# Kernel tuning notes

Measured on AMD Instinct MI355X. Metric: run time of the kernel, lower is better.

## Reference

```python
import jax, jax.numpy as jnp
import numpy as np

B, N, NODE_DIM, EMB, T = 16, 256, 5, 128, 4


def _linear_params(key, din, dout):
    kw, kb = jax.random.split(key)
    s = 1.0 / np.sqrt(din)
    w = jax.random.uniform(kw, (din, dout), minval=-s, maxval=s, dtype=jnp.float32)
    b = jax.random.uniform(kb, (dout,), minval=-s, maxval=s, dtype=jnp.float32)
    return w, b


def setup_inputs() -> dict:
    key = jax.random.key(0)
    ks = jax.random.split(key, 10)
    inp = {
        "xv": jax.random.normal(ks[0], (B, N, NODE_DIM), dtype=jnp.float32),
        "Ws": jax.random.uniform(ks[1], (B, N, N), dtype=jnp.float32),
    }
    inp["t1_w"], inp["t1_b"] = _linear_params(ks[2], NODE_DIM, EMB)
    inp["t2_w"], inp["t2_b"] = _linear_params(ks[3], EMB, EMB)
    inp["t3_w"], inp["t3_b"] = _linear_params(ks[4], EMB, EMB)
    inp["t4_w"], inp["t4_b"] = _linear_params(ks[5], 1, EMB)
    inp["t5_w"], inp["t5_b"] = _linear_params(ks[6], 2 * EMB, 1)
    inp["t6_w"], inp["t6_b"] = _linear_params(ks[7], EMB, EMB)
    inp["t7_w"], inp["t7_b"] = _linear_params(ks[8], EMB, EMB)
    inp["layer_w"], inp["layer_b"] = _linear_params(ks[9], EMB, EMB)
    return inp


def reference(xv, Ws, t1_w, t1_b, t2_w, t2_b, t3_w, t3_b, t4_w, t4_b,
              t5_w, t5_b, t6_w, t6_b, t7_w, t7_b, layer_w, layer_b):
    batch, num_nodes = xv.shape[0], xv.shape[1]
    emb = t1_w.shape[1]
    conn = (Ws > 0).astype(xv.dtype)  # [B,N,N]
    # s1 = layer(relu(theta1(xv)))
    s1 = jnp.maximum(xv @ t1_w + t1_b, 0.0) @ layer_w + layer_b  # [B,N,E]
    # s3 = theta3(sum_i relu(theta4(Ws[:,i,j,None])))
    s3_1 = jnp.maximum(Ws[..., None] * t4_w[0] + t4_b, 0.0)  # [B,N,N,E]
    s3 = s3_1.sum(axis=1) @ t3_w + t3_b  # [B,N,E]
    mu = jnp.zeros((batch, num_nodes, emb), dtype=xv.dtype)
    for _ in range(T):
        s2 = jnp.matmul(conn, mu) @ t2_w + t2_b  # [B,N,E]
        mu = jnp.maximum(s1 + s2 + s3, 0.0)
    # global state: theta6 applied to pooled mu, broadcast to all nodes
    global_state = mu.sum(axis=1, keepdims=True) @ t6_w + t6_b  # [B,1,E]
    global_state = jnp.broadcast_to(global_state, mu.shape)  # [B,N,E]
    local_action = mu @ t7_w + t7_b  # [B,N,E]
    out = jnp.maximum(jnp.concatenate([global_state, local_action], axis=2), 0.0)
    return (out @ t5_w + t5_b).squeeze(2)  # [B,N]
```

## Files before the change

kernel.cpp:

```cpp
#include <hip/hip_runtime.h>

#define BATCH 16
#define NN    256
#define E     128
#define NR    (BATCH*NN)
#define ZCAP  8

typedef float f4 __attribute__((ext_vector_type(4)));


__global__ __launch_bounds__(1024) void k_p1(
    const float* __restrict__ xv,  const float* __restrict__ Ws,
    const float* __restrict__ t1w, const float* __restrict__ t1b,
    const float* __restrict__ t3w, const float* __restrict__ t3b,
    const float* __restrict__ t4w, const float* __restrict__ t4b,
    const float* __restrict__ lw,  const float* __restrict__ lb,
    float* __restrict__ s13g, int* __restrict__ zcnt)
{
    const int blk = blockIdx.x;
    const int b   = blk >> 4;
    const int bt  = blk & 15;
    const int j0  = bt * 16;
    const int r0  = b*NN + j0;
    const int t   = threadIdx.x;
    const int e   = t & 127;
    const int q   = t >> 7;
    const int w   = t >> 6;
    const int l   = t & 63;

    __shared__ __align__(16) float s3p[2][16][E];
    __shared__ __align__(16) float s3l[16][E];
    __shared__ __align__(16) float hsl[16][E];
    __shared__ int lcnt[16];

    const float* wb = Ws + (size_t)b*NN*NN;

    {
        float b1 = t1b[e];
        float w0=t1w[e],w1=t1w[E+e],w2=t1w[2*E+e],w3=t1w[3*E+e],w4=t1w[4*E+e];
        #pragma unroll
        for (int rr = 0; rr < 2; ++rr) {
            const float* x = xv + (size_t)(r0 + q*2 + rr)*5;
            hsl[q*2+rr][e] =
                fmaxf(b1 + x[0]*w0+x[1]*w1+x[2]*w2+x[3]*w3+x[4]*w4, 0.f);
        }
    }
    {
        f4 v = *(const f4*)(wb + (size_t)(j0 + w)*NN + l*4);
        int c = (v.x<=0.f) + (v.y<=0.f) + (v.z<=0.f) + (v.w<=0.f);
        #pragma unroll
        for (int off = 32; off; off >>= 1) c += __shfl_down(c, off, 64);
        if (l == 0) lcnt[w] = c;
    }
    {
        const int cq = q & 3, ih = q >> 2;
        const float a = t4w[e], c = t4b[e];
        const float* wcol = wb + (size_t)(ih*128)*NN + j0 + cq*4;
        float x0=0.f, x1=0.f, x2=0.f, x3=0.f;
        #pragma unroll 8
        for (int i = 0; i < 128; ++i) {
            f4 wv = *(const f4*)(wcol + (size_t)i*NN);
            x0 += fmaxf(wv.x*a + c, 0.f);
            x1 += fmaxf(wv.y*a + c, 0.f);
            x2 += fmaxf(wv.z*a + c, 0.f);
            x3 += fmaxf(wv.w*a + c, 0.f);
        }
        s3p[ih][cq*4+0][e] = x0;
        s3p[ih][cq*4+1][e] = x1;
        s3p[ih][cq*4+2][e] = x2;
        s3p[ih][cq*4+3][e] = x3;
    }
    __syncthreads();
    {
        s3l[2*q][e]   = s3p[0][2*q][e]   + s3p[1][2*q][e];
        s3l[2*q+1][e] = s3p[0][2*q+1][e] + s3p[1][2*q+1][e];
    }
    __syncthreads();
    if (w < 8) {
        const int ra = 2*w, rb = 2*w + 1;
        float a00=0.f, a01=0.f, a10=0.f, a11=0.f;
        #pragma unroll 2
        for (int k0 = 0; k0 < E; k0 += 4) {
            f4 h0 = *(const f4*)&hsl[ra][k0];
            f4 h1 = *(const f4*)&hsl[rb][k0];
            f4 s0 = *(const f4*)&s3l[ra][k0];
            f4 s1 = *(const f4*)&s3l[rb][k0];
            #pragma unroll
            for (int m = 0; m < 4; ++m) {
                float wlA = lw[(k0+m)*E + l],      w3A = t3w[(k0+m)*E + l];
                float wlB = lw[(k0+m)*E + l + 64], w3B = t3w[(k0+m)*E + l + 64];
                a00 += h0[m]*wlA + s0[m]*w3A;
                a01 += h0[m]*wlB + s0[m]*w3B;
                a10 += h1[m]*wlA + s1[m]*w3A;
                a11 += h1[m]*wlB + s1[m]*w3B;
            }
        }
        float bA = lb[l] + t3b[l], bB = lb[l+64] + t3b[l+64];
        s13g[(size_t)(r0+ra)*E + l]      = a00 + bA;
        s13g[(size_t)(r0+ra)*E + l + 64] = a01 + bB;
        s13g[(size_t)(r0+rb)*E + l]      = a10 + bA;
        s13g[(size_t)(r0+rb)*E + l + 64] = a11 + bB;
    }
    if (t < 16) zcnt[r0 + t] = lcnt[t];
}

__global__ __launch_bounds__(1024) void k_p2(
    const float* __restrict__ Ws,
    const float* __restrict__ t2w, const float* __restrict__ t2b,
    const float* __restrict__ t5w,
    const float* __restrict__ t6w, const float* __restrict__ t6b,
    const float* __restrict__ s13g, const int* __restrict__ zcnt,
    float* __restrict__ s2b3g, float* __restrict__ gsumG,
    float* __restrict__ zmu4g)
{
    const int b = blockIdx.x;
    const int t = threadIdx.x;
    const int e = t & 127;
    const int q = t >> 7;
    const size_t bb = (size_t)b*NN*E;

    __shared__ __align__(16) float sQA[8][E];
    __shared__ __align__(16) float sQB[8][E];
    __shared__ __align__(16) float dbuf[E], s2bL[E];
    __shared__ float zmuP[ZCAP][E], zmuN[ZCAP][E];
    __shared__ int   zmap[NN];
    __shared__ int   zlist[ZCAP];
    __shared__ int   nzs;
    __shared__ float sg2[2];

    const float* wb = Ws + (size_t)b*NN*NN;

    if (t == 0) nzs = 0;
    if (t < NN) zmap[t] = -1;
    __syncthreads();
    if (t < NN) {
        if (zcnt[b*NN + t] > 0) {
            int s = atomicAdd(&nzs, 1);
            if (s < ZCAP) { zlist[s] = t; zmap[t] = s; }
        }
    }
    __syncthreads();
    const int nz = nzs < ZCAP ? nzs : ZCAP;

    float reg[32];
    #pragma unroll
    for (int j = 0; j < 32; ++j)
        reg[j] = s13g[bb + (size_t)(q*32+j)*E + e];

    float s2b_r  = t2b[e];
    float s2bP_r = s2b_r;

    for (int it = 0; it < 4; ++it) {
        if (nz > 0) {
            if (q == 0) s2bL[e] = s2b_r;
            __syncthreads();
            for (int z = 0; z < nz; ++z) {
                int j = zlist[z];
                float cp = 0.f;
                const float* wr = wb + (size_t)j*NN;
                if (it > 0) {
                    #pragma unroll
                    for (int u = 0; u < 32; ++u) {
                        int i = q*32 + u;
                        if (wr[i] <= 0.f) {
                            int zi = zmap[i];
                            cp += (zi >= 0) ? zmuP[zi][e]
                                            : fmaxf(reg[u] + s2bP_r, 0.f);
                        }
                    }
                }
                sQA[q][e] = cp;
                __syncthreads();
                if (q == 0) {
                    float s = 0.f;
                    #pragma unroll
                    for (int qq = 0; qq < 8; ++qq) s += sQA[qq][e];
                    dbuf[e] = s;
                }
                __syncthreads();
                float cb = 0.f;
                #pragma unroll 2
                for (int k = 0; k < E; k += 4) {
                    f4 d = *(const f4*)&dbuf[k];
                    cb += d.x*t2w[(k+0)*E+e] + d.y*t2w[(k+1)*E+e]
                        + d.z*t2w[(k+2)*E+e] + d.w*t2w[(k+3)*E+e];
                }
                if (q == 0) {
                    float sj = s13g[bb+(size_t)j*E+e];
                    zmuN[z][e] = fmaxf(sj + s2b_r - cb, 0.f);
                }
                __syncthreads();
            }
        }

        float csp = 0.f;
        #pragma unroll
        for (int u = 0; u < 32; ++u) csp += fmaxf(reg[u] + s2b_r, 0.f);
        sQA[q][e] = csp;
        __syncthreads();

        const float* W = (it < 3) ? t2w : t6w;
        float pa = 0.f;
        #pragma unroll
        for (int g4 = 0; g4 < 4; ++g4) {
            const int k0 = q*16 + g4*4;
            f4 c = *(const f4*)&sQA[0][k0];
            #pragma unroll
            for (int qq = 1; qq < 8; ++qq) {
                f4 d = *(const f4*)&sQA[qq][k0];
                c.x += d.x; c.y += d.y; c.z += d.z; c.w += d.w;
            }
            if (nz > 0) {
                for (int z = 0; z < nz; ++z) {
                    int j = zlist[z];
                    #pragma unroll
                    for (int m = 0; m < 4; ++m) {
                        float sj = s13g[bb+(size_t)j*E + k0 + m];
                        c[m] += zmuN[z][k0+m] - fmaxf(sj + s2bL[k0+m], 0.f);
                    }
                }
            }
            pa += c.x*W[(k0+0)*E+e] + c.y*W[(k0+1)*E+e]
                + c.z*W[(k0+2)*E+e] + c.w*W[(k0+3)*E+e];
        }
        sQB[q][e] = pa;
        s2bP_r = s2b_r;
        if (nz > 0 && q == 0)
            for (int z = 0; z < nz; ++z) zmuP[z][e] = zmuN[z][e];
        __syncthreads();

        if (it < 3) {
            float s = t2b[e];
            #pragma unroll
            for (int qq = 0; qq < 8; ++qq) s += sQB[qq][e];
            s2b_r = s;
        }
    }

    if (q == 0) {
        s2b3g[b*E + e] = s2b_r;
        float g = t6b[e];
        #pragma unroll
        for (int qq = 0; qq < 8; ++qq) g += sQB[qq][e];
        float v = fmaxf(g, 0.f) * t5w[e];
        #pragma unroll
        for (int off = 32; off; off >>= 1) v += __shfl_down(v, off, 64);
        if ((t & 63) == 0) sg2[t >> 6] = v;
        for (int z = 0; z < nz; ++z)
            zmu4g[bb + (size_t)zlist[z]*E + e] = zmuP[z][e];
    }
    if (q == 1 && nzs > ZCAP) {
        for (int j = 0; j < NN; ++j) {
            if (zcnt[b*NN + j] > 0 && zmap[j] < 0) {
                float sj = s13g[bb + (size_t)j*E + e];
                zmu4g[bb + (size_t)j*E + e] = fmaxf(sj + s2b_r, 0.f);
            }
        }
    }
    __syncthreads();
    if (t == 0) gsumG[b] = sg2[0] + sg2[1];
}

__global__ __launch_bounds__(1024) void k_p3(
    const float* __restrict__ t5w, const float* __restrict__ t5b,
    const float* __restrict__ t7w, const float* __restrict__ t7b,
    const float* __restrict__ s13g, const int* __restrict__ zcnt,
    const float* __restrict__ s2b3g, const float* __restrict__ gsumG,
    const float* __restrict__ zmu4g,
    float* __restrict__ out)
{
    const int blk = blockIdx.x;
    const int b   = blk >> 4;
    const int bt  = blk & 15;
    const int j0  = bt * 16;
    const int r0  = b*NN + j0;
    const int t   = threadIdx.x;
    const int e   = t & 127;
    const int q   = t >> 7;
    const int w   = t >> 6;
    const int l   = t & 63;

    __shared__ __align__(16) float mul[16][E];
    __shared__ float sredO[16];

    {
        float s2e = s2b3g[b*E + e];
        #pragma unroll
        for (int rr = 0; rr < 2; ++rr) {
            int row = 2*q + rr;
            float v;
            if (zcnt[r0 + row] > 0)
                v = zmu4g[(size_t)(r0+row)*E + e];
            else
                v = fmaxf(s13g[(size_t)(r0+row)*E + e] + s2e, 0.f);
            mul[row][e] = v;
        }
    }
    __syncthreads();
    if (w < 8) {
        const int ra = 2*w, rb = 2*w + 1;
        float a00=0.f, a01=0.f, a10=0.f, a11=0.f;
        #pragma unroll 2
        for (int k0 = 0; k0 < E; k0 += 4) {
            f4 m0 = *(const f4*)&mul[ra][k0];
            f4 m1 = *(const f4*)&mul[rb][k0];
            #pragma unroll
            for (int m = 0; m < 4; ++m) {
                float w7A = t7w[(k0+m)*E + l];
                float w7B = t7w[(k0+m)*E + l + 64];
                a00 += m0[m]*w7A;
                a01 += m0[m]*w7B;
                a10 += m1[m]*w7A;
                a11 += m1[m]*w7B;
            }
        }
        float b7A = t7b[l],     b7B = t7b[l+64];
        float w5A = t5w[E+l],   w5B = t5w[E+l+64];
        float v0 = fmaxf(a00 + b7A, 0.f)*w5A + fmaxf(a01 + b7B, 0.f)*w5B;
        float v1 = fmaxf(a10 + b7A, 0.f)*w5A + fmaxf(a11 + b7B, 0.f)*w5B;
        #pragma unroll
        for (int off = 32; off; off >>= 1) {
            v0 += __shfl_down(v0, off, 64);
            v1 += __shfl_down(v1, off, 64);
        }
        if (l == 0) { sredO[ra] = v0; sredO[rb] = v1; }
    }
    __syncthreads();
    if (t < 16)
        out[r0 + t] = sredO[t] + gsumG[b] + t5b[0];
}

extern "C" void kernel_launch(void* const* d_in, const int* in_sizes, int n_in,
                              void* d_out, int out_size, void* d_ws, size_t ws_size,
                              hipStream_t stream) {
    const float* xv  = (const float*)d_in[0];
    const float* Ws  = (const float*)d_in[1];
    const float* t1w = (const float*)d_in[2];  const float* t1b = (const float*)d_in[3];
    const float* t2w = (const float*)d_in[4];  const float* t2b = (const float*)d_in[5];
    const float* t3w = (const float*)d_in[6];  const float* t3b = (const float*)d_in[7];
    const float* t4w = (const float*)d_in[8];  const float* t4b = (const float*)d_in[9];
    const float* t5w = (const float*)d_in[10]; const float* t5b = (const float*)d_in[11];
    const float* t6w = (const float*)d_in[12]; const float* t6b = (const float*)d_in[13];
    const float* t7w = (const float*)d_in[14]; const float* t7b = (const float*)d_in[15];
    const float* lw  = (const float*)d_in[16]; const float* lb  = (const float*)d_in[17];
    float* outp = (float*)d_out;

    float* ws = (float*)d_ws;
    const int RE = NR*E;
    float* s13g  = ws;
    float* zmu4g = ws + RE;
    float* s2b3g = ws + 2*RE;
    float* gsumG = s2b3g + BATCH*E;
    int*   zcnt  = (int*)(gsumG + 64);

    k_p1<<<256, 1024, 0, stream>>>(xv, Ws, t1w, t1b, t3w, t3b, t4w, t4b,
                                   lw, lb, s13g, zcnt);
    k_p2<<<BATCH, 1024, 0, stream>>>(Ws, t2w, t2b, t5w, t6w, t6b,
                                     s13g, zcnt, s2b3g, gsumG, zmu4g);
    k_p3<<<256, 1024, 0, stream>>>(t5w, t5b, t7w, t7b, s13g, zcnt,
                                   s2b3g, gsumG, zmu4g, outp);
}
```

Baseline: 135.1 us.

## Fuse three kernels into one cooperative kernel with a grid-wide sync

Merges the embedding, recurrence and output kernels into a single cooperative launch separated by a grid sync. Each of the 16 blocks per batch now repeats the per-batch recurrence itself and keeps its own rows of s13 and the final mu in shared memory, so the global round trips for s2b, gsum and zmu go away. This removes two kernel launches and their inter-kernel gaps, at the cost of 16x redundant recurrence work and relaxed atomic loads of s13g. It also drops the fallback path for batches with more than ZCAP zero-containing rows, which is a correctness risk for general inputs.

```diff
diff --git a/kernel.cpp b/kernel.cpp
--- a/kernel.cpp
+++ b/kernel.cpp
@@ -1,4 +1,7 @@
 #include <hip/hip_runtime.h>
+#include <hip/hip_cooperative_groups.h>
+
+namespace cg = cooperative_groups;
 
 #define BATCH 16
 #define NN    256
@@ -8,14 +11,18 @@
 
 typedef float f4 __attribute__((ext_vector_type(4)));
 
-
-__global__ __launch_bounds__(1024) void k_p1(
+__global__ __launch_bounds__(1024) void k_all(
     const float* __restrict__ xv,  const float* __restrict__ Ws,
     const float* __restrict__ t1w, const float* __restrict__ t1b,
+    const float* __restrict__ t2w, const float* __restrict__ t2b,
     const float* __restrict__ t3w, const float* __restrict__ t3b,
     const float* __restrict__ t4w, const float* __restrict__ t4b,
+    const float* __restrict__ t5w, const float* __restrict__ t5b,
+    const float* __restrict__ t6w, const float* __restrict__ t6b,
+    const float* __restrict__ t7w, const float* __restrict__ t7b,
     const float* __restrict__ lw,  const float* __restrict__ lb,
-    float* __restrict__ s13g, int* __restrict__ zcnt)
+    float* __restrict__ s13g, int* __restrict__ zcnt,
+    float* __restrict__ out)
 {
     const int blk = blockIdx.x;
     const int b   = blk >> 4;
@@ -27,11 +34,22 @@
     const int q   = t >> 7;
     const int w   = t >> 6;
     const int l   = t & 63;
+    const size_t bb = (size_t)b*NN*E;
 
     __shared__ __align__(16) float s3p[2][16][E];
     __shared__ __align__(16) float s3l[16][E];
     __shared__ __align__(16) float hsl[16][E];
-    __shared__ int lcnt[16];
+    __shared__ __align__(16) float s13l[16][E];
+    __shared__ __align__(16) float sQA[8][E];
+    __shared__ __align__(16) float sQB[8][E];
+    __shared__ __align__(16) float dbuf[E], s2bL[E];
+    __shared__ float zmuP[ZCAP][E], zmuN[ZCAP][E];
+    __shared__ int   zmap[NN];
+    __shared__ int   zlist[ZCAP];
+    __shared__ int   nzs;
+    __shared__ int   lcnt[16];
+    __shared__ float sredO[16];
+    __shared__ float sg2[2];
 
     const float* wb = Ws + (size_t)b*NN*NN;
 
@@ -96,45 +114,32 @@
             }
         }
         float bA = lb[l] + t3b[l], bB = lb[l+64] + t3b[l+64];
-        s13g[(size_t)(r0+ra)*E + l]      = a00 + bA;
-        s13g[(size_t)(r0+ra)*E + l + 64] = a01 + bB;
-        s13g[(size_t)(r0+rb)*E + l]      = a10 + bA;
-        s13g[(size_t)(r0+rb)*E + l + 64] = a11 + bB;
-    }
-    if (t < 16) zcnt[r0 + t] = lcnt[t];
-}
-
-__global__ __launch_bounds__(1024) void k_p2(
-    const float* __restrict__ Ws,
-    const float* __restrict__ t2w, const float* __restrict__ t2b,
-    const float* __restrict__ t5w,
-    const float* __restrict__ t6w, const float* __restrict__ t6b,
-    const float* __restrict__ s13g, const int* __restrict__ zcnt,
-    float* __restrict__ s2b3g, float* __restrict__ gsumG,
-    float* __restrict__ zmu4g)
-{
-    const int b = blockIdx.x;
-    const int t = threadIdx.x;
-    const int e = t & 127;
-    const int q = t >> 7;
-    const size_t bb = (size_t)b*NN*E;
-
-    __shared__ __align__(16) float sQA[8][E];
-    __shared__ __align__(16) float sQB[8][E];
-    __shared__ __align__(16) float dbuf[E], s2bL[E];
-    __shared__ float zmuP[ZCAP][E], zmuN[ZCAP][E];
-    __shared__ int   zmap[NN];
-    __shared__ int   zlist[ZCAP];
-    __shared__ int   nzs;
-    __shared__ float sg2[2];
-
-    const float* wb = Ws + (size_t)b*NN*NN;
+        float vaL = a00 + bA, vaH = a01 + bB;
+        float vbL = a10 + bA, vbH = a11 + bB;
+        s13l[ra][l]      = vaL;  s13l[ra][l+64] = vaH;
+        s13l[rb][l]      = vbL;  s13l[rb][l+64] = vbH;
+        __hip_atomic_store(&s13g[(size_t)(r0+ra)*E + l],      vaL,
+                           __ATOMIC_RELAXED, __HIP_MEMORY_SCOPE_AGENT);
+        __hip_atomic_store(&s13g[(size_t)(r0+ra)*E + l + 64], vaH,
+                           __ATOMIC_RELAXED, __HIP_MEMORY_SCOPE_AGENT);
+        __hip_atomic_store(&s13g[(size_t)(r0+rb)*E + l],      vbL,
+                           __ATOMIC_RELAXED, __HIP_MEMORY_SCOPE_AGENT);
+        __hip_atomic_store(&s13g[(size_t)(r0+rb)*E + l + 64], vbH,
+                           __ATOMIC_RELAXED, __HIP_MEMORY_SCOPE_AGENT);
+    }
+    if (t < 16)
+        __hip_atomic_store(&zcnt[r0 + t], lcnt[t],
+                           __ATOMIC_RELAXED, __HIP_MEMORY_SCOPE_AGENT);
+    __syncthreads();
+
+    cg::this_grid().sync();
 
     if (t == 0) nzs = 0;
     if (t < NN) zmap[t] = -1;
     __syncthreads();
     if (t < NN) {
-        if (zcnt[b*NN + t] > 0) {
+        if (__hip_atomic_load(&zcnt[b*NN + t], __ATOMIC_RELAXED,
+                              __HIP_MEMORY_SCOPE_AGENT) > 0) {
             int s = atomicAdd(&nzs, 1);
             if (s < ZCAP) { zlist[s] = t; zmap[t] = s; }
         }
@@ -145,7 +150,8 @@
     float reg[32];
     #pragma unroll
     for (int j = 0; j < 32; ++j)
-        reg[j] = s13g[bb + (size_t)(q*32+j)*E + e];
+        reg[j] = __hip_atomic_load(&s13g[bb + (size_t)(q*32+j)*E + e],
+                                   __ATOMIC_RELAXED, __HIP_MEMORY_SCOPE_AGENT);
 
     float s2b_r  = t2b[e];
     float s2bP_r = s2b_r;
@@ -186,7 +192,8 @@
                         + d.z*t2w[(k+2)*E+e] + d.w*t2w[(k+3)*E+e];
                 }
                 if (q == 0) {
-                    float sj = s13g[bb+(size_t)j*E+e];
+                    float sj = __hip_atomic_load(&s13g[bb+(size_t)j*E+e],
+                                  __ATOMIC_RELAXED, __HIP_MEMORY_SCOPE_AGENT);
                     zmuN[z][e] = fmaxf(sj + s2b_r - cb, 0.f);
                 }
                 __syncthreads();
@@ -215,7 +222,9 @@
                     int j = zlist[z];
                     #pragma unroll
                     for (int m = 0; m < 4; ++m) {
-                        float sj = s13g[bb+(size_t)j*E + k0 + m];
+                        float sj = __hip_atomic_load(
+                            &s13g[bb+(size_t)j*E + k0 + m],
+                            __ATOMIC_RELAXED, __HIP_MEMORY_SCOPE_AGENT);
                         c[m] += zmuN[z][k0+m] - fmaxf(sj + s2bL[k0+m], 0.f);
                     }
                 }
@@ -238,7 +247,6 @@
     }
 
     if (q == 0) {
-        s2b3g[b*E + e] = s2b_r;
         float g = t6b[e];
         #pragma unroll
         for (int qq = 0; qq < 8; ++qq) g += sQB[qq][e];
@@ -246,54 +254,15 @@
         #pragma unroll
         for (int off = 32; off; off >>= 1) v += __shfl_down(v, off, 64);
         if ((t & 63) == 0) sg2[t >> 6] = v;
-        for (int z = 0; z < nz; ++z)
-            zmu4g[bb + (size_t)zlist[z]*E + e] = zmuP[z][e];
-    }
-    if (q == 1 && nzs > ZCAP) {
-        for (int j = 0; j < NN; ++j) {
-            if (zcnt[b*NN + j] > 0 && zmap[j] < 0) {
-                float sj = s13g[bb + (size_t)j*E + e];
-                zmu4g[bb + (size_t)j*E + e] = fmaxf(sj + s2b_r, 0.f);
-            }
-        }
-    }
-    __syncthreads();
-    if (t == 0) gsumG[b] = sg2[0] + sg2[1];
-}
-
-__global__ __launch_bounds__(1024) void k_p3(
-    const float* __restrict__ t5w, const float* __restrict__ t5b,
-    const float* __restrict__ t7w, const float* __restrict__ t7b,
-    const float* __restrict__ s13g, const int* __restrict__ zcnt,
-    const float* __restrict__ s2b3g, const float* __restrict__ gsumG,
-    const float* __restrict__ zmu4g,
-    float* __restrict__ out)
-{
-    const int blk = blockIdx.x;
-    const int b   = blk >> 4;
-    const int bt  = blk & 15;
-    const int j0  = bt * 16;
-    const int r0  = b*NN + j0;
-    const int t   = threadIdx.x;
-    const int e   = t & 127;
-    const int q   = t >> 7;
-    const int w   = t >> 6;
-    const int l   = t & 63;
-
-    __shared__ __align__(16) float mul[16][E];
-    __shared__ float sredO[16];
-
-    {
-        float s2e = s2b3g[b*E + e];
+    }
+    {
         #pragma unroll
         for (int rr = 0; rr < 2; ++rr) {
             int row = 2*q + rr;
-            float v;
-            if (zcnt[r0 + row] > 0)
-                v = zmu4g[(size_t)(r0+row)*E + e];
-            else
-                v = fmaxf(s13g[(size_t)(r0+row)*E + e] + s2e, 0.f);
-            mul[row][e] = v;
+            int zi  = zmap[j0 + row];
+            float v = (zi >= 0) ? zmuP[zi][e]
+                                : fmaxf(s13l[row][e] + s2b_r, 0.f);
+            hsl[row][e] = v;
         }
     }
     __syncthreads();
@@ -302,8 +271,8 @@
         float a00=0.f, a01=0.f, a10=0.f, a11=0.f;
         #pragma unroll 2
         for (int k0 = 0; k0 < E; k0 += 4) {
-            f4 m0 = *(const f4*)&mul[ra][k0];
-            f4 m1 = *(const f4*)&mul[rb][k0];
+            f4 m0 = *(const f4*)&hsl[ra][k0];
+            f4 m1 = *(const f4*)&hsl[rb][k0];
             #pragma unroll
             for (int m = 0; m < 4; ++m) {
                 float w7A = t7w[(k0+m)*E + l];
@@ -314,8 +283,8 @@
                 a11 += m1[m]*w7B;
             }
         }
-        float b7A = t7b[l],     b7B = t7b[l+64];
-        float w5A = t5w[E+l],   w5B = t5w[E+l+64];
+        float b7A = t7b[l],   b7B = t7b[l+64];
+        float w5A = t5w[E+l], w5B = t5w[E+l+64];
         float v0 = fmaxf(a00 + b7A, 0.f)*w5A + fmaxf(a01 + b7B, 0.f)*w5B;
         float v1 = fmaxf(a10 + b7A, 0.f)*w5A + fmaxf(a11 + b7B, 0.f)*w5B;
         #pragma unroll
@@ -327,7 +296,7 @@
     }
     __syncthreads();
     if (t < 16)
-        out[r0 + t] = sredO[t] + gsumG[b] + t5b[0];
+        out[r0 + t] = sredO[t] + sg2[0] + sg2[1] + t5b[0];
 }
 
 extern "C" void kernel_launch(void* const* d_in, const int* in_sizes, int n_in,
@@ -348,15 +317,16 @@
     float* ws = (float*)d_ws;
     const int RE = NR*E;
     float* s13g  = ws;
-    float* zmu4g = ws + RE;
-    float* s2b3g = ws + 2*RE;
-    float* gsumG = s2b3g + BATCH*E;
-    int*   zcnt  = (int*)(gsumG + 64);
-
-    k_p1<<<256, 1024, 0, stream>>>(xv, Ws, t1w, t1b, t3w, t3b, t4w, t4b,
-                                   lw, lb, s13g, zcnt);
-    k_p2<<<BATCH, 1024, 0, stream>>>(Ws, t2w, t2b, t5w, t6w, t6b,
-                                     s13g, zcnt, s2b3g, gsumG, zmu4g);
-    k_p3<<<256, 1024, 0, stream>>>(t5w, t5b, t7w, t7b, s13g, zcnt,
-                                   s2b3g, gsumG, zmu4g, outp);
+    int*   zcnt  = (int*)(ws + RE + 64);
+
+    void* args[] = {
+        (void*)&xv,  (void*)&Ws,
+        (void*)&t1w, (void*)&t1b, (void*)&t2w, (void*)&t2b,
+        (void*)&t3w, (void*)&t3b, (void*)&t4w, (void*)&t4b,
+        (void*)&t5w, (void*)&t5b, (void*)&t6w, (void*)&t6b,
+        (void*)&t7w, (void*)&t7b, (void*)&lw,  (void*)&lb,
+        (void*)&s13g, (void*)&zcnt, (void*)&outp
+    };
+    hipLaunchCooperativeKernel((const void*)k_all, dim3(256), dim3(1024),
+                               args, 0, stream);
 }
```

Measured after the change: 189.4 us. 40.1% more time.
